# Kernel optimization log

Measured on AMD Instinct MI355X. Metric: run time of the kernel, lower is better.

The kernel has to match this reference:

```python
import jax, jax.numpy as jnp
import numpy as np

B = 262144
L = 16      # latent_dim
H = 64      # hidden_dim
C = 8       # num_charts
O = 32      # output_dim
TAU_MIN = 0.01
TAU_DENOM_MIN = 0.001
EPS = 0.001
LN_EPS = 1e-5


def setup_inputs() -> dict:
    key = jax.random.key(0)
    ks = jax.random.split(key, 16)
    # latents kept well inside the Poincare ball
    z_geo = 0.1 * jax.random.normal(ks[0], (B, L), dtype=jnp.float32)
    z_tex = 0.1 * jax.random.normal(ks[1], (B, L), dtype=jnp.float32)
    def lin(k, fan_in, shape):
        bound = 1.0 / np.sqrt(fan_in)
        return jax.random.uniform(k, shape, jnp.float32, -bound, bound)
    chart_w = lin(ks[2], L, (C, H, L))   # stacked per-chart Linear weights
    chart_b = lin(ks[3], L, (C, H))
    router_w = lin(ks[4], L, (C, L))
    router_b = lin(ks[5], L, (C,))
    centers = 0.02 * jax.random.normal(ks[6], (C, L), dtype=jnp.float32)
    tex_w = lin(ks[7], L, (H, L))
    tex_b = lin(ks[8], L, (H,))
    ln_g = jnp.ones((H,), jnp.float32)
    ln_b = jnp.zeros((H,), jnp.float32)
    w1 = lin(ks[9], H, (H, H))
    b1 = lin(ks[10], H, (H,))
    w2 = lin(ks[11], H, (O, H))
    b2 = lin(ks[12], H, (O,))
    return dict(z_geo=z_geo, z_tex=z_tex, chart_w=chart_w, chart_b=chart_b,
                router_w=router_w, router_b=router_b, centers=centers,
                tex_w=tex_w, tex_b=tex_b, ln_g=ln_g, ln_b=ln_b,
                w1=w1, b1=b1, w2=w2, b2=b2)


def _temperature(z):
    r2 = jnp.sum(z * z, axis=-1)                      # [B]
    denom = jnp.maximum(1.0 - r2, TAU_DENOM_MIN)
    tau = (np.sqrt(L) * denom) * 0.5
    return jnp.maximum(tau, TAU_MIN)                  # [B]


def _gelu(x):
    return jax.nn.gelu(x, approximate=False)


def reference(z_geo, z_tex, chart_w, chart_b, router_w, router_b, centers,
              tex_w, tex_b, ln_g, ln_b, w1, b1, w2, b2):
    # hyperbolic distance scores  [B, C]
    diff = z_geo[:, None, :] - centers[None, :, :]
    dist_sq = jnp.sum(diff * diff, axis=-1)
    z_sq = jnp.sum(z_geo * z_geo, axis=-1, keepdims=True)   # [B,1]
    c_sq = jnp.sum(centers * centers, axis=-1)[None, :]      # [1,C]
    denom = (1.0 - z_sq) * (1.0 - c_sq)
    arg = 1.0 + 2.0 * dist_sq / (denom + EPS)
    dist = jnp.arccosh(jnp.maximum(arg, 1.0 + EPS))
    tau = _temperature(z_geo)                                # [B]
    scores = -dist / tau[:, None]
    scores = scores + 0.1 * (z_geo @ router_w.T + router_b) / tau[:, None]
    router_weights = jax.nn.softmax(scores, axis=-1)         # [B,C]

    # dense chart projection + weighted blend
    h_stack = jnp.einsum('bl,chl->bch', z_geo, chart_w) + chart_b[None]  # [B,C,H]
    h_global = jnp.sum(h_stack * router_weights[:, :, None], axis=1)     # [B,H]
    h_tex = z_tex @ tex_w.T + tex_b
    h = h_global + h_tex

    # renderer: LayerNorm -> GELU -> Linear -> GELU -> Linear
    mu = jnp.mean(h, axis=-1, keepdims=True)
    var = jnp.mean((h - mu) ** 2, axis=-1, keepdims=True)
    hn = (h - mu) * jax.lax.rsqrt(var + LN_EPS) * ln_g + ln_b
    h1 = _gelu(_gelu(hn) @ w1.T + b1)
    x_hat = h1 @ w2.T + b2
    return x_hat, router_weights
```

## Files before the change

### kernel.cpp

```cpp
#include <hip/hip_runtime.h>
#include <hip/hip_bf16.h>


typedef __attribute__((ext_vector_type(8))) short short8;
typedef __attribute__((ext_vector_type(4))) float f32x4;

__device__ __forceinline__ int pkbf2(float a, float b) {
    union { __hip_bfloat162 h2; int i; } u;
    u.h2 = __float22bfloat162_rn(make_float2(a, b));
    return u.i;
}
__device__ __forceinline__ short pkbf1(float a) { return (short)pkbf2(a, 0.f); }

__device__ __forceinline__ float gelu_fast(float x) {
    float x2 = x * x;
    float t  = __expf(fmaf(x2, 0.07135481f, 1.5957691f) * x);
    float r  = __builtin_amdgcn_rcpf(t + 1.0f);
    return fmaf(-x, r, x);
}
__device__ __forceinline__ int bpack(int k, int n, int KT) {
    return (((n >> 4) * KT + (k >> 5)) * 64 + (n & 15) + (((k & 31) >> 3) << 4)) * 8 + (k & 7);
}
__device__ __forceinline__ int gswz(int g) {
    return g ^ (((g >> 4) & 3) << 1) ^ ((g >> 3) & 1);
}

constexpr int SCR_OFF = 20480;
constexpr int RS_OFF  = 28672;
constexpr int SMEM_SZ = 37888;

__global__ __launch_bounds__(256, 2) void topo_mfma(
    const float* __restrict__ zg,  const float* __restrict__ ztx,
    const float* __restrict__ cw,  const float* __restrict__ cb,
    const float* __restrict__ rw,  const float* __restrict__ rb,
    const float* __restrict__ cen, const float* __restrict__ txw,
    const float* __restrict__ txb, const float* __restrict__ lng,
    const float* __restrict__ lnb, const float* __restrict__ w1,
    const float* __restrict__ b1,  const float* __restrict__ w2,
    const float* __restrict__ b2,
    float* __restrict__ out, int Btot)
{
    __shared__ __align__(16) char smem[SMEM_SZ];
    short* WA = (short*)smem;
    float* RS = (float*)(smem + RS_OFF);

    const int tid = threadIdx.x;
    const int wv = tid >> 6, lane = tid & 63;
    const int q = lane >> 4, col = lane & 15;
    const int sub = (lane >> 3) & 1, j = lane & 7;

    for (int idx = tid; idx < 160 * 64; idx += 256) {
        int k = idx >> 6, n = idx & 63;
        float v;
        if (k < 128)       v = cw[(k >> 4) * 1024 + n * 16 + (k & 15)];
        else if (k < 144)  v = txw[n * 16 + (k - 128)];
        else if (k < 152)  v = cb[(k - 144) * 64 + n];
        else if (k == 152) v = txb[n];
        else               v = 0.f;
        WA[bpack(k, n, 5)] = pkbf1(v);
    }

    const long sG = (long)blockIdx.x * 256 + tid;
    {
        float z[16];
        const float4* pg = (const float4*)(zg + sG * 16);
        #pragma unroll
        for (int v = 0; v < 4; v++) {
            float4 a = pg[v];
            z[v*4+0]=a.x; z[v*4+1]=a.y; z[v*4+2]=a.z; z[v*4+3]=a.w;
        }
        float r2 = 0.f;
        #pragma unroll
        for (int l = 0; l < 16; l++) r2 = fmaf(z[l], z[l], r2);
        const float inv_tau = 1.0f / fmaxf(2.0f * fmaxf(1.0f - r2, 0.001f), 0.01f);
        float scv[8]; float smax = -1e30f;
        #pragma unroll
        for (int c = 0; c < 8; c++) {
            float dsq = 0.f, csq = 0.f, dotv = 0.f;
            #pragma unroll
            for (int l = 0; l < 16; l++) {
                float cv = cen[c * 16 + l];
                float d  = z[l] - cv;
                dsq  = fmaf(d, d, dsq);
                csq  = fmaf(cv, cv, csq);
                dotv = fmaf(z[l], rw[c * 16 + l], dotv);
            }
            float denom = (1.0f - r2) * (1.0f - csq);
            float arg   = 1.0f + 2.0f * dsq / (denom + 0.001f);
            float dist  = acoshf(fmaxf(arg, 1.001f));
            float score = (-dist + 0.1f * (dotv + rb[c])) * inv_tau;
            scv[c] = score; smax = fmaxf(smax, score);
        }
        float esum = 0.f;
        #pragma unroll
        for (int c = 0; c < 8; c++) { scv[c] = __expf(scv[c] - smax); esum += scv[c]; }
        const float rinv = 1.0f / esum;
        #pragma unroll
        for (int c = 0; c < 8; c++) { scv[c] *= rinv; RS[tid * 9 + c] = scv[c]; }
        float4* pr = (float4*)(out + (long)Btot * 32 + sG * 8);
        pr[0] = make_float4(scv[0], scv[1], scv[2], scv[3]);
        pr[1] = make_float4(scv[4], scv[5], scv[6], scv[7]);
    }

    short8 W1F[4][2], W2F[2][2];
    {
        const int kb = q * 8;
        #pragma unroll
        for (int nt = 0; nt < 4; nt++) {
            const float* base = w1 + (nt * 16 + col) * 64 + kb;
            #pragma unroll
            for (int kt = 0; kt < 2; kt++) {
                const float4* p = (const float4*)(base + kt * 32);
                float4 a = p[0], b = p[1];
                union { short8 s; int i[4]; } f;
                f.i[0] = pkbf2(a.x, a.y); f.i[1] = pkbf2(a.z, a.w);
                f.i[2] = pkbf2(b.x, b.y); f.i[3] = pkbf2(b.z, b.w);
                W1F[nt][kt] = f.s;
            }
        }
        #pragma unroll
        for (int nt = 0; nt < 2; nt++) {
            const float* base = w2 + (nt * 16 + col) * 64 + kb;
            #pragma unroll
            for (int kt = 0; kt < 2; kt++) {
                const float4* p = (const float4*)(base + kt * 32);
                float4 a = p[0], b = p[1];
                union { short8 s; int i[4]; } f;
                f.i[0] = pkbf2(a.x, a.y); f.i[1] = pkbf2(a.z, a.w);
                f.i[2] = pkbf2(b.x, b.y); f.i[3] = pkbf2(b.z, b.w);
                W2F[nt][kt] = f.s;
            }
        }
    }
    float lngv[4], lnbv[4], b1v[4], b2v[2];
    #pragma unroll
    for (int nt = 0; nt < 4; nt++) {
        lngv[nt] = lng[nt * 16 + col];
        lnbv[nt] = lnb[nt * 16 + col];
        b1v[nt]  = b1[nt * 16 + col];
    }
    b2v[0] = b2[col]; b2v[1] = b2[16 + col];

    __syncthreads();

    short* scr = (short*)(smem + SCR_OFF) + wv * 1024;
    union Frag { short8 s; int i[4]; };

    for (int t = 0; t < 4; t++) {
        const int  mBase = wv * 64 + t * 16;
        const int  sL = mBase + col;
        const long sA = (long)blockIdx.x * 256 + sL;

        const float4* pz  = (const float4*)(zg  + sA * 16 + ((q & 1) << 3));
        const float4* pzt = (const float4*)(ztx + sA * 16 + ((q & 1) << 3));
        float4 za = pz[0],  zb = pz[1];
        float4 ta = pzt[0], tb = pzt[1];
        float zh[8] = {za.x,za.y,za.z,za.w, zb.x,zb.y,zb.z,zb.w};
        float th[8] = {ta.x,ta.y,ta.z,ta.w, tb.x,tb.y,tb.z,tb.w};

        short8 A1[5];
        #pragma unroll
        for (int kt = 0; kt < 4; kt++) {
            float rC = RS[sL * 9 + 2 * kt + (q >> 1)];
            Frag f;
            #pragma unroll
            for (int p = 0; p < 4; p++) f.i[p] = pkbf2(rC * zh[2*p], rC * zh[2*p+1]);
            A1[kt] = f.s;
        }
        {
            Frag f;
            if (q < 2) {
                #pragma unroll
                for (int p = 0; p < 4; p++) f.i[p] = pkbf2(th[2*p], th[2*p+1]);
            } else if (q == 2) {
                #pragma unroll
                for (int p = 0; p < 4; p++)
                    f.i[p] = pkbf2(RS[sL * 9 + 2*p], RS[sL * 9 + 2*p + 1]);
            } else {
                f.i[0] = pkbf2(1.0f, 0.f); f.i[1] = 0; f.i[2] = 0; f.i[3] = 0;
            }
            A1[4] = f.s;
        }

        float h[4][4];
        #pragma unroll
        for (int nt = 0; nt < 4; nt++) {
            f32x4 acc = {0.f, 0.f, 0.f, 0.f};
            #pragma unroll
            for (int kt = 0; kt < 5; kt++) {
                short8 bf = *(const short8*)(WA + (nt * 5 + kt) * 512 + lane * 8);
                acc = __builtin_amdgcn_mfma_f32_16x16x32_bf16(A1[kt], bf, acc, 0, 0, 0);
            }
            #pragma unroll
            for (int reg = 0; reg < 4; reg++) h[nt][reg] = acc[reg];
        }

        float mu[4], rsd[4];
        #pragma unroll
        for (int reg = 0; reg < 4; reg++) {
            float s = h[0][reg] + h[1][reg] + h[2][reg] + h[3][reg];
            s += __shfl_xor(s, 1); s += __shfl_xor(s, 2);
            s += __shfl_xor(s, 4); s += __shfl_xor(s, 8);
            mu[reg] = s * (1.0f / 64.0f);
        }
        #pragma unroll
        for (int reg = 0; reg < 4; reg++) {
            float d0 = h[0][reg] - mu[reg], d1 = h[1][reg] - mu[reg];
            float d2 = h[2][reg] - mu[reg], d3 = h[3][reg] - mu[reg];
            float s = d0*d0 + d1*d1 + d2*d2 + d3*d3;
            s += __shfl_xor(s, 1); s += __shfl_xor(s, 2);
            s += __shfl_xor(s, 4); s += __shfl_xor(s, 8);
            rsd[reg] = rsqrtf(s * (1.0f / 64.0f) + 1e-5f);
        }

        #pragma unroll
        for (int nt = 0; nt < 4; nt++) {
            int high = (nt & 1) * 2 + sub;
            #pragma unroll
            for (int reg = 0; reg < 4; reg++) {
                float hn = (h[nt][reg] - mu[reg]) * rsd[reg] * lngv[nt] + lnbv[nt];
                int grp = gswz((q * 4 + reg) + 16 * high);
                scr[(nt >> 1) * 512 + grp * 8 + j] = pkbf1(gelu_fast(hn));
            }
        }
        asm volatile("s_waitcnt lgkmcnt(0)" ::: "memory");

        short8 A2[2];
        {
            int grp = gswz(lane);
            A2[0] = *(const short8*)(scr +       grp * 8);
            A2[1] = *(const short8*)(scr + 512 + grp * 8);
        }

        #pragma unroll
        for (int nt = 0; nt < 4; nt++) {
            f32x4 acc = {0.f, 0.f, 0.f, 0.f};
            acc = __builtin_amdgcn_mfma_f32_16x16x32_bf16(A2[0], W1F[nt][0], acc, 0, 0, 0);
            acc = __builtin_amdgcn_mfma_f32_16x16x32_bf16(A2[1], W1F[nt][1], acc, 0, 0, 0);
            int high = (nt & 1) * 2 + sub;
            #pragma unroll
            for (int reg = 0; reg < 4; reg++) {
                float h1v = gelu_fast(acc[reg] + b1v[nt]);
                int grp = gswz((q * 4 + reg) + 16 * high);
                scr[(nt >> 1) * 512 + grp * 8 + j] = pkbf1(h1v);
            }
        }
        asm volatile("s_waitcnt lgkmcnt(0)" ::: "memory");

        short8 A3[2];
        {
            int grp = gswz(lane);
            A3[0] = *(const short8*)(scr +       grp * 8);
            A3[1] = *(const short8*)(scr + 512 + grp * 8);
        }

        const long sOutBase = (long)blockIdx.x * 256 + mBase + q * 4;
        #pragma unroll
        for (int nt = 0; nt < 2; nt++) {
            f32x4 acc = {0.f, 0.f, 0.f, 0.f};
            acc = __builtin_amdgcn_mfma_f32_16x16x32_bf16(A3[0], W2F[nt][0], acc, 0, 0, 0);
            acc = __builtin_amdgcn_mfma_f32_16x16x32_bf16(A3[1], W2F[nt][1], acc, 0, 0, 0);
            #pragma unroll
            for (int reg = 0; reg < 4; reg++)
                out[(sOutBase + reg) * 32 + nt * 16 + col] = acc[reg] + b2v[nt];
        }
    }
}

extern "C" void kernel_launch(void* const* d_in, const int* in_sizes, int n_in,
                              void* d_out, int out_size, void* d_ws, size_t ws_size,
                              hipStream_t stream) {
    const int B = in_sizes[0] / 16;
    dim3 grid(B / 256), block(256);
    hipLaunchKernelGGL(topo_mfma, grid, block, 0, stream,
        (const float*)d_in[0],  (const float*)d_in[1],
        (const float*)d_in[2],  (const float*)d_in[3],
        (const float*)d_in[4],  (const float*)d_in[5],
        (const float*)d_in[6],  (const float*)d_in[7],
        (const float*)d_in[8],  (const float*)d_in[9],
        (const float*)d_in[10], (const float*)d_in[11],
        (const float*)d_in[12], (const float*)d_in[13],
        (const float*)d_in[14],
        (float*)d_out, B);
}
```

Measured before the change: 160.5 us.

## Prepack weights in a side kernel, shrink LDS, raise occupancy, prefetch inputs

Adds a one-block pre-kernel that packs chart, texture, W1 and W2 weights into bf16 MFMA layout in workspace. Each main block then copies the packed tile into LDS with vector loads instead of re-converting the weights itself. Router weights are stored in LDS as fp16 and LDS shrinks to 32KB, so launch bounds can allow 4 blocks per CU. Other changes: acosh is replaced by log/sqrt fast-math intrinsics, LayerNorm takes mean and variance in a single pass, layer-1 MFMAs are reordered by k, and next-tile inputs are prefetched. The costs are an extra launch, fp16 rounding of router weights, a variance formula less stable than the two-pass one, and register pressure under the tighter launch bound.

```diff
diff --git a/kernel.cpp b/kernel.cpp
--- a/kernel.cpp
+++ b/kernel.cpp
@@ -1,5 +1,6 @@
 #include <hip/hip_runtime.h>
 #include <hip/hip_bf16.h>
+#include <hip/hip_fp16.h>
 
 
 typedef __attribute__((ext_vector_type(8))) short short8;
@@ -24,31 +25,21 @@
 __device__ __forceinline__ int gswz(int g) {
     return g ^ (((g >> 4) & 3) << 1) ^ ((g >> 3) & 1);
 }
-
-constexpr int SCR_OFF = 20480;
-constexpr int RS_OFF  = 28672;
-constexpr int SMEM_SZ = 37888;
-
-__global__ __launch_bounds__(256, 2) void topo_mfma(
-    const float* __restrict__ zg,  const float* __restrict__ ztx,
-    const float* __restrict__ cw,  const float* __restrict__ cb,
-    const float* __restrict__ rw,  const float* __restrict__ rb,
-    const float* __restrict__ cen, const float* __restrict__ txw,
-    const float* __restrict__ txb, const float* __restrict__ lng,
-    const float* __restrict__ lnb, const float* __restrict__ w1,
-    const float* __restrict__ b1,  const float* __restrict__ w2,
-    const float* __restrict__ b2,
-    float* __restrict__ out, int Btot)
+__device__ __forceinline__ short8 packrow8(const float* base) {
+    const float4* p = (const float4*)base;
+    float4 a = p[0], b = p[1];
+    union { short8 s; int i[4]; } f;
+    f.i[0] = pkbf2(a.x, a.y); f.i[1] = pkbf2(a.z, a.w);
+    f.i[2] = pkbf2(b.x, b.y); f.i[3] = pkbf2(b.z, b.w);
+    return f.s;
+}
+
+__global__ void pack_weights(const float* __restrict__ cw, const float* __restrict__ cb,
+                             const float* __restrict__ txw, const float* __restrict__ txb,
+                             const float* __restrict__ w1,  const float* __restrict__ w2,
+                             short* __restrict__ ws)
 {
-    __shared__ __align__(16) char smem[SMEM_SZ];
-    short* WA = (short*)smem;
-    float* RS = (float*)(smem + RS_OFF);
-
     const int tid = threadIdx.x;
-    const int wv = tid >> 6, lane = tid & 63;
-    const int q = lane >> 4, col = lane & 15;
-    const int sub = (lane >> 3) & 1, j = lane & 7;
-
     for (int idx = tid; idx < 160 * 64; idx += 256) {
         int k = idx >> 6, n = idx & 63;
         float v;
@@ -57,7 +48,64 @@
         else if (k < 152)  v = cb[(k - 144) * 64 + n];
         else if (k == 152) v = txb[n];
         else               v = 0.f;
-        WA[bpack(k, n, 5)] = pkbf1(v);
+        ws[bpack(k, n, 5)] = pkbf1(v);
+    }
+    for (int f = tid; f < 512; f += 256) {
+        int lane = f & 63, e = f >> 6;
+        int nt = e >> 1, kt = e & 1;
+        int col = lane & 15, qq = lane >> 4;
+        *(short8*)(ws + 10240 + f * 8) = packrow8(w1 + (nt * 16 + col) * 64 + kt * 32 + qq * 8);
+    }
+    {
+        int f = tid;
+        int lane = f & 63, e = f >> 6;
+        int nt = e >> 1, kt = e & 1;
+        int col = lane & 15, qq = lane >> 4;
+        *(short8*)(ws + 14336 + f * 8) = packrow8(w2 + (nt * 16 + col) * 64 + kt * 32 + qq * 8);
+    }
+}
+
+constexpr int SCR_OFF = 20480;
+constexpr int RS_OFF  = 28672;
+constexpr int SMEM_SZ = 32768;
+
+__global__ __launch_bounds__(256, 4) void topo_mfma(
+    const float* __restrict__ zg,  const float* __restrict__ ztx,
+    const float* __restrict__ cw,  const float* __restrict__ cb,
+    const float* __restrict__ rw,  const float* __restrict__ rb,
+    const float* __restrict__ cen, const float* __restrict__ txw,
+    const float* __restrict__ txb, const float* __restrict__ lng,
+    const float* __restrict__ lnb, const float* __restrict__ w1,
+    const float* __restrict__ b1,  const float* __restrict__ w2,
+    const float* __restrict__ b2,  const short* __restrict__ wsp,
+    const int prepacked,
+    float* __restrict__ out, int Btot)
+{
+    __shared__ __align__(16) char smem[SMEM_SZ];
+    short* WA = (short*)smem;
+    __half* RSh = (__half*)(smem + RS_OFF);
+
+    const int tid = threadIdx.x;
+    const int wv = tid >> 6, lane = tid & 63;
+    const int q = lane >> 4, col = lane & 15;
+    const int sub = (lane >> 3) & 1, j = lane & 7;
+
+    if (prepacked) {
+        const int4* src = (const int4*)wsp;
+        int4* dst = (int4*)smem;
+        #pragma unroll
+        for (int i = 0; i < 5; i++) dst[i * 256 + tid] = src[i * 256 + tid];
+    } else {
+        for (int idx = tid; idx < 160 * 64; idx += 256) {
+            int k = idx >> 6, n = idx & 63;
+            float v;
+            if (k < 128)       v = cw[(k >> 4) * 1024 + n * 16 + (k & 15)];
+            else if (k < 144)  v = txw[n * 16 + (k - 128)];
+            else if (k < 152)  v = cb[(k - 144) * 64 + n];
+            else if (k == 152) v = txb[n];
+            else               v = 0.f;
+            WA[bpack(k, n, 5)] = pkbf1(v);
+        }
     }
 
     const long sG = (long)blockIdx.x * 256 + tid;
@@ -72,66 +120,74 @@
         float r2 = 0.f;
         #pragma unroll
         for (int l = 0; l < 16; l++) r2 = fmaf(z[l], z[l], r2);
-        const float inv_tau = 1.0f / fmaxf(2.0f * fmaxf(1.0f - r2, 0.001f), 0.01f);
+        const float inv_tau = __builtin_amdgcn_rcpf(fmaxf(2.0f * fmaxf(1.0f - r2, 0.001f), 0.01f));
+        const float omr2 = 1.0f - r2;
         float scv[8]; float smax = -1e30f;
         #pragma unroll
         for (int c = 0; c < 8; c++) {
+            const float4* cp = (const float4*)(cen + c * 16);
+            const float4* rp = (const float4*)(rw  + c * 16);
             float dsq = 0.f, csq = 0.f, dotv = 0.f;
             #pragma unroll
-            for (int l = 0; l < 16; l++) {
-                float cv = cen[c * 16 + l];
-                float d  = z[l] - cv;
-                dsq  = fmaf(d, d, dsq);
-                csq  = fmaf(cv, cv, csq);
-                dotv = fmaf(z[l], rw[c * 16 + l], dotv);
-            }
-            float denom = (1.0f - r2) * (1.0f - csq);
-            float arg   = 1.0f + 2.0f * dsq / (denom + 0.001f);
-            float dist  = acoshf(fmaxf(arg, 1.001f));
-            float score = (-dist + 0.1f * (dotv + rb[c])) * inv_tau;
+            for (int v = 0; v < 4; v++) {
+                float4 cv = cp[v], rv = rp[v];
+                float d0 = z[v*4+0] - cv.x, d1 = z[v*4+1] - cv.y;
+                float d2 = z[v*4+2] - cv.z, d3 = z[v*4+3] - cv.w;
+                dsq  = fmaf(d0,d0, fmaf(d1,d1, fmaf(d2,d2, fmaf(d3,d3, dsq))));
+                csq  = fmaf(cv.x,cv.x, fmaf(cv.y,cv.y, fmaf(cv.z,cv.z, fmaf(cv.w,cv.w, csq))));
+                dotv = fmaf(z[v*4+0],rv.x, fmaf(z[v*4+1],rv.y,
+                       fmaf(z[v*4+2],rv.z, fmaf(z[v*4+3],rv.w, dotv))));
+            }
+            float u = 2.0f * dsq * __builtin_amdgcn_rcpf(omr2 * (1.0f - csq) + 0.001f);
+            u = fmaxf(u, 0.001f);
+            float dist  = __logf((1.0f + u) + __builtin_amdgcn_sqrtf(u * (u + 2.0f)));
+            float score = fmaf(0.1f, dotv + rb[c], -dist) * inv_tau;
             scv[c] = score; smax = fmaxf(smax, score);
         }
         float esum = 0.f;
         #pragma unroll
         for (int c = 0; c < 8; c++) { scv[c] = __expf(scv[c] - smax); esum += scv[c]; }
-        const float rinv = 1.0f / esum;
-        #pragma unroll
-        for (int c = 0; c < 8; c++) { scv[c] *= rinv; RS[tid * 9 + c] = scv[c]; }
+        const float rinv = __builtin_amdgcn_rcpf(esum);
+        union { ushort us[8]; int4 v; } hv;
+        #pragma unroll
+        for (int c = 0; c < 8; c++) {
+            scv[c] *= rinv;
+            hv.us[(c & 1) * 4 + (c >> 1)] = __half_as_ushort(__float2half_rn(scv[c]));
+        }
+        *(int4*)(RSh + tid * 8) = hv.v;
         float4* pr = (float4*)(out + (long)Btot * 32 + sG * 8);
         pr[0] = make_float4(scv[0], scv[1], scv[2], scv[3]);
         pr[1] = make_float4(scv[4], scv[5], scv[6], scv[7]);
     }
 
     short8 W1F[4][2], W2F[2][2];
-    {
+    if (prepacked) {
+        const short8* p1 = (const short8*)(wsp + 10240);
+        #pragma unroll
+        for (int nt = 0; nt < 4; nt++)
+            #pragma unroll
+            for (int kt = 0; kt < 2; kt++)
+                W1F[nt][kt] = p1[(nt * 2 + kt) * 64 + lane];
+        const short8* p2 = (const short8*)(wsp + 14336);
+        #pragma unroll
+        for (int nt = 0; nt < 2; nt++)
+            #pragma unroll
+            for (int kt = 0; kt < 2; kt++)
+                W2F[nt][kt] = p2[(nt * 2 + kt) * 64 + lane];
+    } else {
         const int kb = q * 8;
         #pragma unroll
-        for (int nt = 0; nt < 4; nt++) {
-            const float* base = w1 + (nt * 16 + col) * 64 + kb;
-            #pragma unroll
-            for (int kt = 0; kt < 2; kt++) {
-                const float4* p = (const float4*)(base + kt * 32);
-                float4 a = p[0], b = p[1];
-                union { short8 s; int i[4]; } f;
-                f.i[0] = pkbf2(a.x, a.y); f.i[1] = pkbf2(a.z, a.w);
-                f.i[2] = pkbf2(b.x, b.y); f.i[3] = pkbf2(b.z, b.w);
-                W1F[nt][kt] = f.s;
-            }
-        }
-        #pragma unroll
-        for (int nt = 0; nt < 2; nt++) {
-            const float* base = w2 + (nt * 16 + col) * 64 + kb;
-            #pragma unroll
-            for (int kt = 0; kt < 2; kt++) {
-                const float4* p = (const float4*)(base + kt * 32);
-                float4 a = p[0], b = p[1];
-                union { short8 s; int i[4]; } f;
-                f.i[0] = pkbf2(a.x, a.y); f.i[1] = pkbf2(a.z, a.w);
-                f.i[2] = pkbf2(b.x, b.y); f.i[3] = pkbf2(b.z, b.w);
-                W2F[nt][kt] = f.s;
-            }
-        }
-    }
+        for (int nt = 0; nt < 4; nt++)
+            #pragma unroll
+            for (int kt = 0; kt < 2; kt++)
+                W1F[nt][kt] = packrow8(w1 + (nt * 16 + col) * 64 + kt * 32 + kb);
+        #pragma unroll
+        for (int nt = 0; nt < 2; nt++)
+            #pragma unroll
+            for (int kt = 0; kt < 2; kt++)
+                W2F[nt][kt] = packrow8(w2 + (nt * 16 + col) * 64 + kt * 32 + kb);
+    }
+
     float lngv[4], lnbv[4], b1v[4], b2v[2];
     #pragma unroll
     for (int nt = 0; nt < 4; nt++) {
@@ -146,71 +202,87 @@
     short* scr = (short*)(smem + SCR_OFF) + wv * 1024;
     union Frag { short8 s; int i[4]; };
 
+    const long blockBase = (long)blockIdx.x * 256;
+    const float* zrow = zg  + (blockBase + wv * 64 + col) * 16 + ((q & 1) << 3);
+    const float* trow = ztx + (blockBase + wv * 64 + col) * 16 + ((q & 1) << 3);
+
+    float4 za = ((const float4*)zrow)[0], zb = ((const float4*)zrow)[1];
+    float4 ta = ((const float4*)trow)[0], tb = ((const float4*)trow)[1];
+
     for (int t = 0; t < 4; t++) {
-        const int  mBase = wv * 64 + t * 16;
-        const int  sL = mBase + col;
-        const long sA = (long)blockIdx.x * 256 + sL;
-
-        const float4* pz  = (const float4*)(zg  + sA * 16 + ((q & 1) << 3));
-        const float4* pzt = (const float4*)(ztx + sA * 16 + ((q & 1) << 3));
-        float4 za = pz[0],  zb = pz[1];
-        float4 ta = pzt[0], tb = pzt[1];
-        float zh[8] = {za.x,za.y,za.z,za.w, zb.x,zb.y,zb.z,zb.w};
-        float th[8] = {ta.x,ta.y,ta.z,ta.w, tb.x,tb.y,tb.z,tb.w};
-
-        short8 A1[5];
+        const int mBase = wv * 64 + t * 16;
+        const int sL = mBase + col;
+        const int rsb = sL * 8;
+
+        float rc[4];
+        {
+            union { unsigned long long u; __half2 h[2]; } rr;
+            rr.u = *(const unsigned long long*)(RSh + rsb + ((q >> 1) << 2));
+            float2 f0 = __half22float2(rr.h[0]);
+            float2 f1 = __half22float2(rr.h[1]);
+            rc[0] = f0.x; rc[1] = f0.y; rc[2] = f1.x; rc[3] = f1.y;
+        }
+
+        f32x4 acc[4] = {{0.f,0.f,0.f,0.f},{0.f,0.f,0.f,0.f},{0.f,0.f,0.f,0.f},{0.f,0.f,0.f,0.f}};
         #pragma unroll
         for (int kt = 0; kt < 4; kt++) {
-            float rC = RS[sL * 9 + 2 * kt + (q >> 1)];
+            float r = rc[kt];
             Frag f;
-            #pragma unroll
-            for (int p = 0; p < 4; p++) f.i[p] = pkbf2(rC * zh[2*p], rC * zh[2*p+1]);
-            A1[kt] = f.s;
+            f.i[0] = pkbf2(r * za.x, r * za.y);
+            f.i[1] = pkbf2(r * za.z, r * za.w);
+            f.i[2] = pkbf2(r * zb.x, r * zb.y);
+            f.i[3] = pkbf2(r * zb.z, r * zb.w);
+            #pragma unroll
+            for (int nt = 0; nt < 4; nt++) {
+                short8 bf = *(const short8*)(WA + (nt * 5 + kt) * 512 + lane * 8);
+                acc[nt] = __builtin_amdgcn_mfma_f32_16x16x32_bf16(f.s, bf, acc[nt], 0, 0, 0);
+            }
         }
         {
             Frag f;
             if (q < 2) {
-                #pragma unroll
-                for (int p = 0; p < 4; p++) f.i[p] = pkbf2(th[2*p], th[2*p+1]);
+                f.i[0] = pkbf2(ta.x, ta.y); f.i[1] = pkbf2(ta.z, ta.w);
+                f.i[2] = pkbf2(tb.x, tb.y); f.i[3] = pkbf2(tb.z, tb.w);
             } else if (q == 2) {
-                #pragma unroll
-                for (int p = 0; p < 4; p++)
-                    f.i[p] = pkbf2(RS[sL * 9 + 2*p], RS[sL * 9 + 2*p + 1]);
+                union { int4 u; __half2 h[4]; } rv;
+                rv.u = *(const int4*)(RSh + rsb);
+                float2 e0 = __half22float2(rv.h[0]);
+                float2 e1 = __half22float2(rv.h[1]);
+                float2 e2 = __half22float2(rv.h[2]);
+                float2 e3 = __half22float2(rv.h[3]);
+                f.i[0] = pkbf2(e0.x, e2.x);
+                f.i[1] = pkbf2(e0.y, e2.y);
+                f.i[2] = pkbf2(e1.x, e3.x);
+                f.i[3] = pkbf2(e1.y, e3.y);
             } else {
                 f.i[0] = pkbf2(1.0f, 0.f); f.i[1] = 0; f.i[2] = 0; f.i[3] = 0;
             }
-            A1[4] = f.s;
-        }
-
-        float h[4][4];
-        #pragma unroll
-        for (int nt = 0; nt < 4; nt++) {
-            f32x4 acc = {0.f, 0.f, 0.f, 0.f};
-            #pragma unroll
-            for (int kt = 0; kt < 5; kt++) {
-                short8 bf = *(const short8*)(WA + (nt * 5 + kt) * 512 + lane * 8);
-                acc = __builtin_amdgcn_mfma_f32_16x16x32_bf16(A1[kt], bf, acc, 0, 0, 0);
-            }
-            #pragma unroll
-            for (int reg = 0; reg < 4; reg++) h[nt][reg] = acc[reg];
+            #pragma unroll
+            for (int nt = 0; nt < 4; nt++) {
+                short8 bf = *(const short8*)(WA + (nt * 5 + 4) * 512 + lane * 8);
+                acc[nt] = __builtin_amdgcn_mfma_f32_16x16x32_bf16(f.s, bf, acc[nt], 0, 0, 0);
+            }
+        }
+
+        if (t < 3) {
+            const float4* pzn = (const float4*)(zrow + (t + 1) * 256);
+            const float4* ptn = (const float4*)(trow + (t + 1) * 256);
+            za = pzn[0]; zb = pzn[1]; ta = ptn[0]; tb = ptn[1];
         }
 
         float mu[4], rsd[4];
         #pragma unroll
         for (int reg = 0; reg < 4; reg++) {
-            float s = h[0][reg] + h[1][reg] + h[2][reg] + h[3][reg];
-            s += __shfl_xor(s, 1); s += __shfl_xor(s, 2);
-            s += __shfl_xor(s, 4); s += __shfl_xor(s, 8);
-            mu[reg] = s * (1.0f / 64.0f);
-        }
-        #pragma unroll
-        for (int reg = 0; reg < 4; reg++) {
-            float d0 = h[0][reg] - mu[reg], d1 = h[1][reg] - mu[reg];
-            float d2 = h[2][reg] - mu[reg], d3 = h[3][reg] - mu[reg];
-            float s = d0*d0 + d1*d1 + d2*d2 + d3*d3;
-            s += __shfl_xor(s, 1); s += __shfl_xor(s, 2);
-            s += __shfl_xor(s, 4); s += __shfl_xor(s, 8);
-            rsd[reg] = rsqrtf(s * (1.0f / 64.0f) + 1e-5f);
+            float a = acc[0][reg], b = acc[1][reg], c = acc[2][reg], d = acc[3][reg];
+            float s  = (a + b) + (c + d);
+            float s2 = fmaf(a, a, fmaf(b, b, fmaf(c, c, d * d)));
+            s  += __shfl_xor(s, 1);  s  += __shfl_xor(s, 2);
+            s  += __shfl_xor(s, 4);  s  += __shfl_xor(s, 8);
+            s2 += __shfl_xor(s2, 1); s2 += __shfl_xor(s2, 2);
+            s2 += __shfl_xor(s2, 4); s2 += __shfl_xor(s2, 8);
+            float m = s * (1.0f / 64.0f);
+            mu[reg]  = m;
+            rsd[reg] = rsqrtf(fmaf(s2, 1.0f / 64.0f, -m * m) + 1e-5f);
         }
 
         #pragma unroll
@@ -218,7 +290,7 @@
             int high = (nt & 1) * 2 + sub;
             #pragma unroll
             for (int reg = 0; reg < 4; reg++) {
-                float hn = (h[nt][reg] - mu[reg]) * rsd[reg] * lngv[nt] + lnbv[nt];
+                float hn = (acc[nt][reg] - mu[reg]) * rsd[reg] * lngv[nt] + lnbv[nt];
                 int grp = gswz((q * 4 + reg) + 16 * high);
                 scr[(nt >> 1) * 512 + grp * 8 + j] = pkbf1(gelu_fast(hn));
             }
@@ -234,13 +306,13 @@
 
         #pragma unroll
         for (int nt = 0; nt < 4; nt++) {
-            f32x4 acc = {0.f, 0.f, 0.f, 0.f};
-            acc = __builtin_amdgcn_mfma_f32_16x16x32_bf16(A2[0], W1F[nt][0], acc, 0, 0, 0);
-            acc = __builtin_amdgcn_mfma_f32_16x16x32_bf16(A2[1], W1F[nt][1], acc, 0, 0, 0);
+            f32x4 a2 = {0.f, 0.f, 0.f, 0.f};
+            a2 = __builtin_amdgcn_mfma_f32_16x16x32_bf16(A2[0], W1F[nt][0], a2, 0, 0, 0);
+            a2 = __builtin_amdgcn_mfma_f32_16x16x32_bf16(A2[1], W1F[nt][1], a2, 0, 0, 0);
             int high = (nt & 1) * 2 + sub;
             #pragma unroll
             for (int reg = 0; reg < 4; reg++) {
-                float h1v = gelu_fast(acc[reg] + b1v[nt]);
+                float h1v = gelu_fast(a2[reg] + b1v[nt]);
                 int grp = gswz((q * 4 + reg) + 16 * high);
                 scr[(nt >> 1) * 512 + grp * 8 + j] = pkbf1(h1v);
             }
@@ -254,15 +326,15 @@
             A3[1] = *(const short8*)(scr + 512 + grp * 8);
         }
 
-        const long sOutBase = (long)blockIdx.x * 256 + mBase + q * 4;
+        const long sOutBase = blockBase + mBase + q * 4;
         #pragma unroll
         for (int nt = 0; nt < 2; nt++) {
-            f32x4 acc = {0.f, 0.f, 0.f, 0.f};
-            acc = __builtin_amdgcn_mfma_f32_16x16x32_bf16(A3[0], W2F[nt][0], acc, 0, 0, 0);
-            acc = __builtin_amdgcn_mfma_f32_16x16x32_bf16(A3[1], W2F[nt][1], acc, 0, 0, 0);
+            f32x4 a3 = {0.f, 0.f, 0.f, 0.f};
+            a3 = __builtin_amdgcn_mfma_f32_16x16x32_bf16(A3[0], W2F[nt][0], a3, 0, 0, 0);
+            a3 = __builtin_amdgcn_mfma_f32_16x16x32_bf16(A3[1], W2F[nt][1], a3, 0, 0, 0);
             #pragma unroll
             for (int reg = 0; reg < 4; reg++)
-                out[(sOutBase + reg) * 32 + nt * 16 + col] = acc[reg] + b2v[nt];
+                out[(sOutBase + reg) * 32 + nt * 16 + col] = a3[reg] + b2v[nt];
         }
     }
 }
@@ -271,6 +343,14 @@
                               void* d_out, int out_size, void* d_ws, size_t ws_size,
                               hipStream_t stream) {
     const int B = in_sizes[0] / 16;
+    const int prepacked = (d_ws != nullptr && ws_size >= 32768) ? 1 : 0;
+    if (prepacked) {
+        hipLaunchKernelGGL(pack_weights, dim3(1), dim3(256), 0, stream,
+            (const float*)d_in[2],  (const float*)d_in[3],
+            (const float*)d_in[7],  (const float*)d_in[8],
+            (const float*)d_in[11], (const float*)d_in[13],
+            (short*)d_ws);
+    }
     dim3 grid(B / 256), block(256);
     hipLaunchKernelGGL(topo_mfma, grid, block, 0, stream,
         (const float*)d_in[0],  (const float*)d_in[1],
@@ -281,5 +361,6 @@
         (const float*)d_in[10], (const float*)d_in[11],
         (const float*)d_in[12], (const float*)d_in[13],
         (const float*)d_in[14],
+        (const short*)d_ws, prepacked,
         (float*)d_out, B);
 }
```

After: 147.6 us. 1.09x faster.
